# Kernel optimization log

Hardware: AMD Instinct MI355X
Metric: run time of the kernel (lower is better)

The kernel has to match this reference:

```python
import jax, jax.numpy as jnp
import numpy as np

VOCAB = 50257
FEATURES = 128
RESERVOIR = 8
FROZEN_INDEX = 0
B, S = 16, 2048


def setup_inputs() -> dict:
    key = jax.random.key(0)
    k1, k2, k3 = jax.random.split(key, 3)
    base_indices = jax.random.randint(k1, (B, S), 0, VOCAB, dtype=jnp.int64 if jax.config.jax_enable_x64 else jnp.int32)
    reservoir_lookup = jax.random.randint(k2, (VOCAB, RESERVOIR), 0, VOCAB, dtype=jnp.int64 if jax.config.jax_enable_x64 else jnp.int32)
    embedding_weight = jax.random.normal(k3, (VOCAB, FEATURES), dtype=jnp.float32)
    return {"base_indices": base_indices, "reservoir_lookup": reservoir_lookup, "embedding_weight": embedding_weight}


def reference(base_indices, reservoir_lookup, embedding_weight):
    # Zero out the frozen row (value and, via the mask, its gradient --
    # equivalent to the straight-through masking in the torch module).
    vocab = embedding_weight.shape[0]
    mask = (jnp.arange(vocab) != FROZEN_INDEX).astype(embedding_weight.dtype)[:, None]  # [V,1]
    w_eff = embedding_weight * mask                       # [V,F], frozen row = 0
    reservoir_indices = reservoir_lookup[base_indices]    # [B,S,R]
    gathered = w_eff[reservoir_indices]                   # [B,S,R,F]
    return jnp.sum(gathered, axis=-2)                     # [B,S,F]
```

## Files before the change

kernel.cpp:

```cpp
#include <hip/hip_runtime.h>


#define VOCAB 50257
#define FEATURES 128
#define RESERVOIR 8
#define NTOK (16 * 2048)
#define TPG 4

typedef float float4v __attribute__((ext_vector_type(4)));

__global__ __launch_bounds__(256) void reservoir_embed_kernel(
    const int* __restrict__ base_indices,
    const int* __restrict__ reservoir_lookup,
    const float* __restrict__ weight,
    float* __restrict__ out)
{
    const int gid  = blockIdx.x * blockDim.x + threadIdx.x;
    const int grp  = gid >> 5;
    const int lane = gid & 31;
    const int t0   = grp * TPG;

    const int4 b4 = *reinterpret_cast<const int4*>(base_indices + t0);
    const int bases[TPG] = {b4.x, b4.y, b4.z, b4.w};

    int idx[TPG][RESERVOIR];
#pragma unroll
    for (int t = 0; t < TPG; ++t) {
        const int4* rlp = reinterpret_cast<const int4*>(
            reservoir_lookup + bases[t] * RESERVOIR);
        const int4 i0 = rlp[0];
        const int4 i1 = rlp[1];
        idx[t][0] = i0.x; idx[t][1] = i0.y; idx[t][2] = i0.z; idx[t][3] = i0.w;
        idx[t][4] = i1.x; idx[t][5] = i1.y; idx[t][6] = i1.z; idx[t][7] = i1.w;
    }

    float4v acc[TPG];
#pragma unroll
    for (int t = 0; t < TPG; ++t) acc[t] = (float4v){0.f, 0.f, 0.f, 0.f};

#pragma unroll
    for (int t = 0; t < TPG; ++t) {
        float4v rows[RESERVOIR];
#pragma unroll
        for (int r = 0; r < RESERVOIR; ++r) {
            rows[r] = *reinterpret_cast<const float4v*>(
                weight + (((unsigned)idx[t][r]) << 7) + (lane << 2));
        }
#pragma unroll
        for (int r = 0; r < RESERVOIR; ++r) {
            const float m = (idx[t][r] != 0) ? 1.0f : 0.0f;
            acc[t] += m * rows[r];
        }
    }

#pragma unroll
    for (int t = 0; t < TPG; ++t) {
        float4v* op = reinterpret_cast<float4v*>(
            out + (unsigned)(t0 + t) * FEATURES + (lane << 2));
        __builtin_nontemporal_store(acc[t], op);
    }
}

extern "C" void kernel_launch(void* const* d_in, const int* in_sizes, int n_in,
                              void* d_out, int out_size, void* d_ws, size_t ws_size,
                              hipStream_t stream) {
    (void)in_sizes; (void)n_in; (void)out_size; (void)d_ws; (void)ws_size;
    const int*   base_indices     = (const int*)d_in[0];
    const int*   reservoir_lookup = (const int*)d_in[1];
    const float* weight           = (const float*)d_in[2];
    float*       out              = (float*)d_out;

    const int threads = 256;
    const int groups  = NTOK / TPG;
    const int blocks  = groups * 32 / threads;
    reservoir_embed_kernel<<<blocks, threads, 0, stream>>>(
        base_indices, reservoir_lookup, weight, out);
}
```

Before: 24.86 us.

## Sort gathered row indices by vocab slice within each group to improve locality

Each lane now loads one reservoir index, then the 32 indices in a group are ranked by vocab slice using ballots and popcount and scattered through shared memory into slice order. Rows are then gathered in that sorted order and masked into per-token accumulators chosen by a tag packed into the key. The intent is to cluster row fetches by address region for better cache and TLB behaviour, and to spread the index loads across lanes. In exchange it adds a 16-iteration ballot loop, a shared-memory round trip, shuffles and four times as many FMAs per row, plus an occupancy hint in the launch bounds.

```diff
diff --git a/kernel.cpp b/kernel.cpp
--- a/kernel.cpp
+++ b/kernel.cpp
@@ -6,58 +6,74 @@
 #define RESERVOIR 8
 #define NTOK (16 * 2048)
 #define TPG 4
+#define SLICE_SHIFT 12
 
 typedef float float4v __attribute__((ext_vector_type(4)));
 
-__global__ __launch_bounds__(256) void reservoir_embed_kernel(
+__global__ __launch_bounds__(256, 4) void reservoir_embed_kernel(
     const int* __restrict__ base_indices,
     const int* __restrict__ reservoir_lookup,
     const float* __restrict__ weight,
     float* __restrict__ out)
 {
-    const int gid  = blockIdx.x * blockDim.x + threadIdx.x;
+    const int tid  = threadIdx.x;
+    const int gid  = blockIdx.x * 256 + tid;
     const int grp  = gid >> 5;
     const int lane = gid & 31;
+    const int half = (tid >> 5) & 1;
     const int t0   = grp * TPG;
 
-    const int4 b4 = *reinterpret_cast<const int4*>(base_indices + t0);
-    const int bases[TPG] = {b4.x, b4.y, b4.z, b4.w};
+    const int t = lane >> 3;
+    const int r = lane & 7;
+    const int base  = base_indices[t0 + t];
+    const int myidx = reservoir_lookup[base * RESERVOIR + r];
 
-    int idx[TPG][RESERVOIR];
-#pragma unroll
-    for (int t = 0; t < TPG; ++t) {
-        const int4* rlp = reinterpret_cast<const int4*>(
-            reservoir_lookup + bases[t] * RESERVOIR);
-        const int4 i0 = rlp[0];
-        const int4 i1 = rlp[1];
-        idx[t][0] = i0.x; idx[t][1] = i0.y; idx[t][2] = i0.z; idx[t][3] = i0.w;
-        idx[t][4] = i1.x; idx[t][5] = i1.y; idx[t][6] = i1.z; idx[t][7] = i1.w;
+    const int s = myidx >> SLICE_SHIFT;
+    const unsigned below = (1u << lane) - 1u;
+    int rank = 0;
+    for (int k = 0; k < 16; ++k) {
+        unsigned long long b = __ballot(s == k);
+        unsigned m = (unsigned)(b >> (half * 32));
+        if (k < s)       rank += __popc(m);
+        else if (k == s) rank += __popc(m & below);
     }
+
+    const int key = (myidx << 2) | t;
+    __shared__ int smem[256];
+    smem[(tid & ~31) + rank] = key;
+    const int skey = smem[tid];
 
     float4v acc[TPG];
 #pragma unroll
-    for (int t = 0; t < TPG; ++t) acc[t] = (float4v){0.f, 0.f, 0.f, 0.f};
+    for (int i = 0; i < TPG; ++i) acc[i] = (float4v){0.f, 0.f, 0.f, 0.f};
 
 #pragma unroll
-    for (int t = 0; t < TPG; ++t) {
-        float4v rows[RESERVOIR];
+    for (int b = 0; b < 2; ++b) {
+        int keys[16];
+        float4v rows[16];
 #pragma unroll
-        for (int r = 0; r < RESERVOIR; ++r) {
-            rows[r] = *reinterpret_cast<const float4v*>(
-                weight + (((unsigned)idx[t][r]) << 7) + (lane << 2));
+        for (int i = 0; i < 16; ++i) {
+            keys[i] = __shfl(skey, b * 16 + i, 32);
+            const float* p = weight + (((unsigned)keys[i] >> 2) << 7) + (lane << 2);
+            rows[i] = *reinterpret_cast<const float4v*>(p);
         }
 #pragma unroll
-        for (int r = 0; r < RESERVOIR; ++r) {
-            const float m = (idx[t][r] != 0) ? 1.0f : 0.0f;
-            acc[t] += m * rows[r];
+        for (int i = 0; i < 16; ++i) {
+            const int kk = keys[i];
+            const int tt = kk & 3;
+            const float m = ((kk >> 2) != 0) ? 1.0f : 0.0f;
+            acc[0] += ((tt == 0) ? m : 0.0f) * rows[i];
+            acc[1] += ((tt == 1) ? m : 0.0f) * rows[i];
+            acc[2] += ((tt == 2) ? m : 0.0f) * rows[i];
+            acc[3] += ((tt == 3) ? m : 0.0f) * rows[i];
         }
     }
 
 #pragma unroll
-    for (int t = 0; t < TPG; ++t) {
+    for (int i = 0; i < TPG; ++i) {
         float4v* op = reinterpret_cast<float4v*>(
-            out + (unsigned)(t0 + t) * FEATURES + (lane << 2));
-        __builtin_nontemporal_store(acc[t], op);
+            out + (unsigned)(t0 + i) * FEATURES + (lane << 2));
+        __builtin_nontemporal_store(acc[i], op);
     }
 }
 
```

After: 24.15 us. -2.9%, faster.

## Sort gathered row indices per group and pipeline row loads with block barriers

Applied to the files above, without the earlier changes.

Each lane now loads one (token, reservoir) index, and the 32 keys in a group are sorted with a warp bitonic network so rows are visited in ascending address order. Rows are then streamed through a depth-4 register queue that is refilled by broadcasting the next key with a shuffle. Each row is added into the accumulator of the token it belongs to. Periodic __syncthreads calls are added, apparently to keep wavefronts roughly in step so they share cache locality. The change trades the earlier fully unrolled set of independent loads for sort and shuffle overhead, fewer loads in flight, and barrier stalls. It also sets a minimum blocks-per-SM hint in the launch bounds.

```diff
diff --git a/kernel.cpp b/kernel.cpp
--- a/kernel.cpp
+++ b/kernel.cpp
@@ -6,58 +6,82 @@
 #define RESERVOIR 8
 #define NTOK (16 * 2048)
 #define TPG 4
+#define NPAIR 32
+#define DEPTH 4
 
 typedef float float4v __attribute__((ext_vector_type(4)));
 
-__global__ __launch_bounds__(256) void reservoir_embed_kernel(
+__global__ __launch_bounds__(256, 4) void reservoir_embed_kernel(
     const int* __restrict__ base_indices,
     const int* __restrict__ reservoir_lookup,
     const float* __restrict__ weight,
     float* __restrict__ out)
 {
-    const int gid  = blockIdx.x * blockDim.x + threadIdx.x;
+    const int tid  = threadIdx.x;
+    const int gid  = blockIdx.x * 256 + tid;
     const int grp  = gid >> 5;
     const int lane = gid & 31;
     const int t0   = grp * TPG;
 
-    const int4 b4 = *reinterpret_cast<const int4*>(base_indices + t0);
-    const int bases[TPG] = {b4.x, b4.y, b4.z, b4.w};
+    const int t_own = lane >> 3;
+    const int r_own = lane & 7;
+    const int base  = base_indices[t0 + t_own];
+    const int myidx = reservoir_lookup[base * RESERVOIR + r_own];
 
-    int idx[TPG][RESERVOIR];
+    int key = (myidx << 3) | t_own;
+
 #pragma unroll
-    for (int t = 0; t < TPG; ++t) {
-        const int4* rlp = reinterpret_cast<const int4*>(
-            reservoir_lookup + bases[t] * RESERVOIR);
-        const int4 i0 = rlp[0];
-        const int4 i1 = rlp[1];
-        idx[t][0] = i0.x; idx[t][1] = i0.y; idx[t][2] = i0.z; idx[t][3] = i0.w;
-        idx[t][4] = i1.x; idx[t][5] = i1.y; idx[t][6] = i1.z; idx[t][7] = i1.w;
+    for (int m = 2; m <= 32; m <<= 1) {
+#pragma unroll
+        for (int s = m >> 1; s >= 1; s >>= 1) {
+            const int partner = __shfl_xor(key, s, 32);
+            const bool asc    = ((lane & m) == 0);
+            const bool lower  = ((lane & s) == 0);
+            const int mn = min(key, partner);
+            const int mx = max(key, partner);
+            key = (lower == asc) ? mn : mx;
+        }
     }
 
     float4v acc[TPG];
 #pragma unroll
-    for (int t = 0; t < TPG; ++t) acc[t] = (float4v){0.f, 0.f, 0.f, 0.f};
+    for (int j = 0; j < TPG; ++j) acc[j] = (float4v){0.f, 0.f, 0.f, 0.f};
 
+    int     kq[DEPTH];
+    float4v rq[DEPTH];
 #pragma unroll
-    for (int t = 0; t < TPG; ++t) {
-        float4v rows[RESERVOIR];
-#pragma unroll
-        for (int r = 0; r < RESERVOIR; ++r) {
-            rows[r] = *reinterpret_cast<const float4v*>(
-                weight + (((unsigned)idx[t][r]) << 7) + (lane << 2));
-        }
-#pragma unroll
-        for (int r = 0; r < RESERVOIR; ++r) {
-            const float m = (idx[t][r] != 0) ? 1.0f : 0.0f;
-            acc[t] += m * rows[r];
-        }
+    for (int k = 0; k < DEPTH; ++k) {
+        kq[k] = __shfl(key, k, 32);
+        rq[k] = *reinterpret_cast<const float4v*>(
+            weight + (((unsigned)kq[k] >> 3) << 7) + (lane << 2));
     }
 
 #pragma unroll
-    for (int t = 0; t < TPG; ++t) {
+    for (int k = 0; k < NPAIR; ++k) {
+        const int     q   = k & (DEPTH - 1);
+        const int     ck  = kq[q];
+        const float4v row = rq[q];
+        if (k + DEPTH < NPAIR) {
+            const int nk = __shfl(key, k + DEPTH, 32);
+            kq[q] = nk;
+            rq[q] = *reinterpret_cast<const float4v*>(
+                weight + (((unsigned)nk >> 3) << 7) + (lane << 2));
+        }
+        const float m  = ((ck >> 3) != 0) ? 1.0f : 0.0f;
+        const int   tt = ck & 7;
+#pragma unroll
+        for (int j = 0; j < TPG; ++j) {
+            const float mj = (tt == j) ? m : 0.0f;
+            acc[j] += mj * row;
+        }
+        if ((k & 7) == 7 && k + 1 < NPAIR) __syncthreads();
+    }
+
+#pragma unroll
+    for (int j = 0; j < TPG; ++j) {
         float4v* op = reinterpret_cast<float4v*>(
-            out + (unsigned)(t0 + t) * FEATURES + (lane << 2));
-        __builtin_nontemporal_store(acc[t], op);
+            out + (unsigned)(t0 + j) * FEATURES + (lane << 2));
+        __builtin_nontemporal_store(acc[j], op);
     }
 }
 
```

Measured after the change: 24.04 us. -3.3%, faster.
